# Kernel tuning notes

Measured on AMD Instinct MI355X. Metric: run time of the kernel, lower is better.

Reference implementation:

```python
import jax, jax.numpy as jnp
import numpy as np

B, T, E, H = 8, 2048, 1024, 64

def setup_inputs() -> dict:
    key = jax.random.key(0)
    kx, kq, kk, kv = jax.random.split(key, 4)
    x = jax.random.normal(kx, (B, T, E), dtype=jnp.float32)
    # torch Linear(E, H, bias=False): weight [H, E]; store transposed [E, H]
    scale = 1.0 / np.sqrt(E)
    Wq = jax.random.uniform(kq, (E, H), dtype=jnp.float32, minval=-scale, maxval=scale)
    Wk = jax.random.uniform(kk, (E, H), dtype=jnp.float32, minval=-scale, maxval=scale)
    Wv = jax.random.uniform(kv, (E, H), dtype=jnp.float32, minval=-scale, maxval=scale)
    return {"x": x, "Wq": Wq, "Wk": Wk, "Wv": Wv}

def reference(x, Wq, Wk, Wv):
    # x: [B,T,E]
    q = x @ Wq  # [B,T,H]
    k = x @ Wk
    v = x @ Wv
    head_size = q.shape[-1]
    scores = jnp.einsum('bth,bsh->bts', q, k) * (head_size ** -0.5)  # [B,T,T]
    Tlen = x.shape[1]
    causal = jnp.tril(jnp.ones((Tlen, Tlen), dtype=bool))
    scores = jnp.where(causal, scores, -jnp.inf)
    weights = jax.nn.softmax(scores, axis=-1)
    # dropout p=0.0 -> identity
    out = jnp.einsum('bts,bsh->bth', weights, v)  # [B,T,H]
    return out
```

## Files before the change

### kernel.cpp

```cpp
#include <hip/hip_runtime.h>
#include <hip/hip_bf16.h>

#define B_  8
#define T_  2048
#define E_  1024
#define H_  64
#define BT_ (B_*T_)

typedef __attribute__((ext_vector_type(8))) __bf16 bf16x8;
typedef __attribute__((ext_vector_type(4))) float  f32x4;

__device__ __forceinline__ unsigned short f2bfu(float f) {
    union { float f; unsigned u; } v; v.f = f;
    unsigned r = v.u + 0x7fffu + ((v.u >> 16) & 1u);
    return (unsigned short)(r >> 16);
}

__global__ __launch_bounds__(256, 2)
void qkv_kernel(const float* __restrict__ x,
                const float* __restrict__ Wq,
                const float* __restrict__ Wk,
                const float* __restrict__ Wv,
                unsigned short* __restrict__ qb,
                unsigned short* __restrict__ kb,
                unsigned short* __restrict__ vtb)
{
    __shared__ unsigned short xs[64 * 40];
    __shared__ unsigned short wt[3][64 * 40];

    const int tid  = threadIdx.x;
    const int wave = tid >> 6;
    const int lane = tid & 63;
    const int quad = lane >> 4;
    const int col  = lane & 15;
    const long r0  = (long)blockIdx.x * 64;

    f32x4 acc[3][4];
#pragma unroll
    for (int m = 0; m < 3; ++m)
#pragma unroll
        for (int n = 0; n < 4; ++n)
            acc[m][n] = (f32x4){0.f, 0.f, 0.f, 0.f};

    const float* W[3] = {Wq, Wk, Wv};

    const int xrow = tid >> 2;
    const int xk   = (tid & 3) * 8;
    const int wk   = tid >> 3;
    const int wh   = (tid & 7) * 8;

    for (int k0 = 0; k0 < E_; k0 += 32) {
        const float* xp = x + (r0 + xrow) * E_ + k0 + xk;
        float4 f0 = ((const float4*)xp)[0];
        float4 f1 = ((const float4*)xp)[1];
        unsigned pack[4];
        pack[0] = f2bfu(f0.x) | ((unsigned)f2bfu(f0.y) << 16);
        pack[1] = f2bfu(f0.z) | ((unsigned)f2bfu(f0.w) << 16);
        pack[2] = f2bfu(f1.x) | ((unsigned)f2bfu(f1.y) << 16);
        pack[3] = f2bfu(f1.z) | ((unsigned)f2bfu(f1.w) << 16);

        float wg[3][8];
#pragma unroll
        for (int m = 0; m < 3; ++m) {
            const float* wp = W[m] + (long)(k0 + wk) * H_ + wh;
            float4 g0 = ((const float4*)wp)[0];
            float4 g1 = ((const float4*)wp)[1];
            wg[m][0]=g0.x; wg[m][1]=g0.y; wg[m][2]=g0.z; wg[m][3]=g0.w;
            wg[m][4]=g1.x; wg[m][5]=g1.y; wg[m][6]=g1.z; wg[m][7]=g1.w;
        }

        __syncthreads();

        *(uint4*)&xs[xrow * 40 + xk] = *(uint4*)pack;
#pragma unroll
        for (int m = 0; m < 3; ++m)
#pragma unroll
            for (int j = 0; j < 8; ++j)
                wt[m][(wh + j) * 40 + wk] = f2bfu(wg[m][j]);

        __syncthreads();

        bf16x8 af = *(const bf16x8*)&xs[(wave * 16 + col) * 40 + quad * 8];
#pragma unroll
        for (int m = 0; m < 3; ++m)
#pragma unroll
            for (int n = 0; n < 4; ++n) {
                bf16x8 bfg = *(const bf16x8*)&wt[m][(n * 16 + col) * 40 + quad * 8];
                acc[m][n] = __builtin_amdgcn_mfma_f32_16x16x32_bf16(af, bfg, acc[m][n], 0, 0, 0);
            }
    }

    const int bidx = (int)(r0 >> 11);
#pragma unroll
    for (int n = 0; n < 4; ++n) {
        int h = n * 16 + col;
#pragma unroll
        for (int r = 0; r < 4; ++r) {
            long t = r0 + wave * 16 + quad * 4 + r;
            qb[t * H_ + h] = f2bfu(acc[0][n][r] * 0.125f);
            kb[t * H_ + h] = f2bfu(acc[1][n][r]);
            vtb[((long)(bidx * H_ + h)) * T_ + (t & (T_ - 1))] = f2bfu(acc[2][n][r]);
        }
    }
}

#define TS 72

__global__ __launch_bounds__(256, 2)
void attn_kernel(const unsigned short* __restrict__ qb,
                 const unsigned short* __restrict__ kb,
                 const unsigned short* __restrict__ vtb,
                 float* __restrict__ out)
{
    __shared__ unsigned short qs[64 * TS];
    __shared__ unsigned short ks[64 * TS];
    __shared__ unsigned short vs[64 * TS];
    __shared__ unsigned short ps[4][16 * TS];

    const int tid  = threadIdx.x;
    const int wave = tid >> 6;
    const int lane = tid & 63;
    const int quad = lane >> 4;
    const int col  = lane & 15;
    const int qt   = blockIdx.x & 31;
    const int b    = blockIdx.x >> 5;

    {
        const uint4* src = (const uint4*)(qb + ((long)b * T_ + qt * 64) * H_);
#pragma unroll
        for (int i = 0; i < 2; ++i) {
            int idx = tid + i * 256;
            int row = idx >> 3, c = idx & 7;
            *(uint4*)&qs[row * TS + c * 8] = src[idx];
        }
    }

    f32x4 o[4];
    float m_i[4], l_i[4];
#pragma unroll
    for (int n = 0; n < 4; ++n) o[n] = (f32x4){0.f, 0.f, 0.f, 0.f};
#pragma unroll
    for (int r = 0; r < 4; ++r) { m_i[r] = -1e30f; l_i[r] = 0.f; }

    for (int s = 0; s <= qt; ++s) {
        {
            const uint4* ksrc = (const uint4*)(kb + ((long)b * T_ + s * 64) * H_);
#pragma unroll
            for (int i = 0; i < 2; ++i) {
                int idx = tid + i * 256;
                int row = idx >> 3, c = idx & 7;
                *(uint4*)&ks[row * TS + c * 8] = ksrc[idx];
                const uint4* vsrc =
                    (const uint4*)(vtb + ((long)(b * H_ + row)) * T_ + s * 64) + c;
                *(uint4*)&vs[row * TS + c * 8] = *vsrc;
            }
        }
        __syncthreads();

        bf16x8 qa0 = *(const bf16x8*)&qs[(wave * 16 + col) * TS + quad * 8];
        bf16x8 qa1 = *(const bf16x8*)&qs[(wave * 16 + col) * TS + quad * 8 + 32];
        f32x4 sa[4];
#pragma unroll
        for (int kt = 0; kt < 4; ++kt) {
            bf16x8 kf0 = *(const bf16x8*)&ks[(kt * 16 + col) * TS + quad * 8];
            bf16x8 kf1 = *(const bf16x8*)&ks[(kt * 16 + col) * TS + quad * 8 + 32];
            sa[kt] = (f32x4){0.f, 0.f, 0.f, 0.f};
            sa[kt] = __builtin_amdgcn_mfma_f32_16x16x32_bf16(qa0, kf0, sa[kt], 0, 0, 0);
            sa[kt] = __builtin_amdgcn_mfma_f32_16x16x32_bf16(qa1, kf1, sa[kt], 0, 0, 0);
        }

        if (s == qt) {
#pragma unroll
            for (int kt = 0; kt < 4; ++kt) {
                int kg = kt * 16 + col;
#pragma unroll
                for (int r = 0; r < 4; ++r) {
                    int qg = wave * 16 + quad * 4 + r;
                    if (kg > qg) sa[kt][r] = -1e30f;
                }
            }
        }

        float mx[4];
#pragma unroll
        for (int r = 0; r < 4; ++r)
            mx[r] = fmaxf(fmaxf(sa[0][r], sa[1][r]), fmaxf(sa[2][r], sa[3][r]));
#pragma unroll
        for (int off = 1; off < 16; off <<= 1)
#pragma unroll
            for (int r = 0; r < 4; ++r)
                mx[r] = fmaxf(mx[r], __shfl_xor(mx[r], off, 64));

        float alpha[4], mnew[4];
#pragma unroll
        for (int r = 0; r < 4; ++r) {
            mnew[r]  = fmaxf(m_i[r], mx[r]);
            alpha[r] = __builtin_amdgcn_exp2f((m_i[r] - mnew[r]) * 1.44269504f);
            m_i[r]   = mnew[r];
        }

        float rs[4] = {0.f, 0.f, 0.f, 0.f};
#pragma unroll
        for (int kt = 0; kt < 4; ++kt)
#pragma unroll
            for (int r = 0; r < 4; ++r) {
                float p = __builtin_amdgcn_exp2f((sa[kt][r] - mnew[r]) * 1.44269504f);
                rs[r] += p;
                ps[wave][(quad * 4 + r) * TS + kt * 16 + col] = f2bfu(p);
            }
#pragma unroll
        for (int off = 1; off < 16; off <<= 1)
#pragma unroll
            for (int r = 0; r < 4; ++r)
                rs[r] += __shfl_xor(rs[r], off, 64);
#pragma unroll
        for (int r = 0; r < 4; ++r)
            l_i[r] = l_i[r] * alpha[r] + rs[r];

#pragma unroll
        for (int n = 0; n < 4; ++n)
#pragma unroll
            for (int r = 0; r < 4; ++r)
                o[n][r] *= alpha[r];

        bf16x8 pa0 = *(const bf16x8*)&ps[wave][col * TS + quad * 8];
        bf16x8 pa1 = *(const bf16x8*)&ps[wave][col * TS + quad * 8 + 32];
#pragma unroll
        for (int n = 0; n < 4; ++n) {
            bf16x8 vf0 = *(const bf16x8*)&vs[(n * 16 + col) * TS + quad * 8];
            bf16x8 vf1 = *(const bf16x8*)&vs[(n * 16 + col) * TS + quad * 8 + 32];
            o[n] = __builtin_amdgcn_mfma_f32_16x16x32_bf16(pa0, vf0, o[n], 0, 0, 0);
            o[n] = __builtin_amdgcn_mfma_f32_16x16x32_bf16(pa1, vf1, o[n], 0, 0, 0);
        }
        __syncthreads();
    }

#pragma unroll
    for (int r = 0; r < 4; ++r) {
        float inv = 1.0f / l_i[r];
        long row = (long)b * T_ + qt * 64 + wave * 16 + quad * 4 + r;
#pragma unroll
        for (int n = 0; n < 4; ++n)
            out[row * H_ + n * 16 + col] = o[n][r] * inv;
    }
}

extern "C" void kernel_launch(void* const* d_in, const int* in_sizes, int n_in,
                              void* d_out, int out_size, void* d_ws, size_t ws_size,
                              hipStream_t stream) {
    (void)in_sizes; (void)n_in; (void)out_size; (void)ws_size;
    const float* x  = (const float*)d_in[0];
    const float* Wq = (const float*)d_in[1];
    const float* Wk = (const float*)d_in[2];
    const float* Wv = (const float*)d_in[3];

    unsigned short* qb  = (unsigned short*)d_ws;
    unsigned short* kb  = qb + (size_t)BT_ * H_;
    unsigned short* vtb = kb + (size_t)BT_ * H_;

    qkv_kernel<<<BT_ / 64, 256, 0, stream>>>(x, Wq, Wk, Wv, qb, kb, vtb);
    attn_kernel<<<B_ * (T_ / 64), 256, 0, stream>>>(qb, kb, vtb, (float*)d_out);
}
```

Before: 195.7 us.

## Pre-convert weights to bf16, shrink QKV and attention tiles for more blocks

Result: slower. 245.5 us (+25.4%).

```diff
diff --git a/kernel.cpp b/kernel.cpp
--- a/kernel.cpp
+++ b/kernel.cpp
@@ -16,120 +16,104 @@
     return (unsigned short)(r >> 16);
 }
 
-__global__ __launch_bounds__(256, 2)
+__global__ __launch_bounds__(256)
+void wprep_kernel(const float* __restrict__ Wq,
+                  const float* __restrict__ Wk,
+                  const float* __restrict__ Wv,
+                  unsigned short* __restrict__ wtb)
+{
+    const int mat = blockIdx.x >> 6;
+    const int h   = blockIdx.x & 63;
+    const float* W = (mat == 0) ? Wq : (mat == 1 ? Wk : Wv);
+    unsigned short* row = wtb + ((long)(mat * 64 + h)) * E_;
+    const int e0 = threadIdx.x * 4;
+    unsigned p0 = f2bfu(W[(e0 + 0) * H_ + h]) | ((unsigned)f2bfu(W[(e0 + 1) * H_ + h]) << 16);
+    unsigned p1 = f2bfu(W[(e0 + 2) * H_ + h]) | ((unsigned)f2bfu(W[(e0 + 3) * H_ + h]) << 16);
+    *(uint2*)&row[e0] = (uint2){p0, p1};
+}
+
+__global__ __launch_bounds__(256, 4)
 void qkv_kernel(const float* __restrict__ x,
-                const float* __restrict__ Wq,
-                const float* __restrict__ Wk,
-                const float* __restrict__ Wv,
+                const unsigned short* __restrict__ wtb,
                 unsigned short* __restrict__ qb,
                 unsigned short* __restrict__ kb,
                 unsigned short* __restrict__ vtb)
 {
-    __shared__ unsigned short xs[64 * 40];
-    __shared__ unsigned short wt[3][64 * 40];
+    __shared__ unsigned short xs[2][16 * 72];
 
     const int tid  = threadIdx.x;
     const int wave = tid >> 6;
     const int lane = tid & 63;
     const int quad = lane >> 4;
     const int col  = lane & 15;
-    const long r0  = (long)blockIdx.x * 64;
-
-    f32x4 acc[3][4];
-#pragma unroll
-    for (int m = 0; m < 3; ++m)
-#pragma unroll
-        for (int n = 0; n < 4; ++n)
-            acc[m][n] = (f32x4){0.f, 0.f, 0.f, 0.f};
-
-    const float* W[3] = {Wq, Wk, Wv};
-
-    const int xrow = tid >> 2;
-    const int xk   = (tid & 3) * 8;
-    const int wk   = tid >> 3;
-    const int wh   = (tid & 7) * 8;
-
-    for (int k0 = 0; k0 < E_; k0 += 32) {
-        const float* xp = x + (r0 + xrow) * E_ + k0 + xk;
-        float4 f0 = ((const float4*)xp)[0];
-        float4 f1 = ((const float4*)xp)[1];
-        unsigned pack[4];
-        pack[0] = f2bfu(f0.x) | ((unsigned)f2bfu(f0.y) << 16);
-        pack[1] = f2bfu(f0.z) | ((unsigned)f2bfu(f0.w) << 16);
-        pack[2] = f2bfu(f1.x) | ((unsigned)f2bfu(f1.y) << 16);
-        pack[3] = f2bfu(f1.z) | ((unsigned)f2bfu(f1.w) << 16);
-
-        float wg[3][8];
-#pragma unroll
-        for (int m = 0; m < 3; ++m) {
-            const float* wp = W[m] + (long)(k0 + wk) * H_ + wh;
-            float4 g0 = ((const float4*)wp)[0];
-            float4 g1 = ((const float4*)wp)[1];
-            wg[m][0]=g0.x; wg[m][1]=g0.y; wg[m][2]=g0.z; wg[m][3]=g0.w;
-            wg[m][4]=g1.x; wg[m][5]=g1.y; wg[m][6]=g1.z; wg[m][7]=g1.w;
-        }
-
+    const long r0  = (long)blockIdx.x * 16;
+
+    f32x4 acc[3];
+#pragma unroll
+    for (int m = 0; m < 3; ++m) acc[m] = (f32x4){0.f, 0.f, 0.f, 0.f};
+
+    const int xrow = tid >> 4;
+    const int xkc  = (tid & 15) * 4;
+    const float* xbase = x + (r0 + xrow) * E_ + xkc;
+
+    float4 xv = *(const float4*)xbase;
+
+    for (int k0 = 0, it = 0; k0 < E_; k0 += 64, ++it) {
+        unsigned p0 = f2bfu(xv.x) | ((unsigned)f2bfu(xv.y) << 16);
+        unsigned p1 = f2bfu(xv.z) | ((unsigned)f2bfu(xv.w) << 16);
+        *(uint2*)&xs[it & 1][xrow * 72 + xkc] = (uint2){p0, p1};
         __syncthreads();
-
-        *(uint4*)&xs[xrow * 40 + xk] = *(uint4*)pack;
-#pragma unroll
-        for (int m = 0; m < 3; ++m)
-#pragma unroll
-            for (int j = 0; j < 8; ++j)
-                wt[m][(wh + j) * 40 + wk] = f2bfu(wg[m][j]);
-
-        __syncthreads();
-
-        bf16x8 af = *(const bf16x8*)&xs[(wave * 16 + col) * 40 + quad * 8];
-#pragma unroll
-        for (int m = 0; m < 3; ++m)
-#pragma unroll
-            for (int n = 0; n < 4; ++n) {
-                bf16x8 bfg = *(const bf16x8*)&wt[m][(n * 16 + col) * 40 + quad * 8];
-                acc[m][n] = __builtin_amdgcn_mfma_f32_16x16x32_bf16(af, bfg, acc[m][n], 0, 0, 0);
-            }
+        if (k0 + 64 < E_) xv = *(const float4*)(xbase + k0 + 64);
+
+#pragma unroll
+        for (int ks = 0; ks < 2; ++ks) {
+            bf16x8 af = *(const bf16x8*)&xs[it & 1][col * 72 + ks * 32 + quad * 8];
+            const int kk = k0 + ks * 32 + quad * 8;
+#pragma unroll
+            for (int m = 0; m < 3; ++m) {
+                bf16x8 bfg = *(const bf16x8*)&wtb[((long)(m * 64 + wave * 16 + col)) * E_ + kk];
+                acc[m] = __builtin_amdgcn_mfma_f32_16x16x32_bf16(af, bfg, acc[m], 0, 0, 0);
+            }
+        }
     }
 
     const int bidx = (int)(r0 >> 11);
-#pragma unroll
-    for (int n = 0; n < 4; ++n) {
-        int h = n * 16 + col;
-#pragma unroll
-        for (int r = 0; r < 4; ++r) {
-            long t = r0 + wave * 16 + quad * 4 + r;
-            qb[t * H_ + h] = f2bfu(acc[0][n][r] * 0.125f);
-            kb[t * H_ + h] = f2bfu(acc[1][n][r]);
-            vtb[((long)(bidx * H_ + h)) * T_ + (t & (T_ - 1))] = f2bfu(acc[2][n][r]);
-        }
+    const int h    = wave * 16 + col;
+#pragma unroll
+    for (int r = 0; r < 4; ++r) {
+        long t = r0 + quad * 4 + r;
+        qb[t * H_ + h] = f2bfu(acc[0][r] * 0.125f);
+        kb[t * H_ + h] = f2bfu(acc[1][r]);
+        vtb[((long)(bidx * H_ + h)) * T_ + (t & (T_ - 1))] = f2bfu(acc[2][r]);
     }
 }
 
 #define TS 72
 
-__global__ __launch_bounds__(256, 2)
+__global__ __launch_bounds__(128, 4)
 void attn_kernel(const unsigned short* __restrict__ qb,
                  const unsigned short* __restrict__ kb,
                  const unsigned short* __restrict__ vtb,
                  float* __restrict__ out)
 {
-    __shared__ unsigned short qs[64 * TS];
+    __shared__ unsigned short qs[32 * TS];
     __shared__ unsigned short ks[64 * TS];
     __shared__ unsigned short vs[64 * TS];
-    __shared__ unsigned short ps[4][16 * TS];
+    __shared__ unsigned short ps[2][16 * TS];
 
     const int tid  = threadIdx.x;
     const int wave = tid >> 6;
     const int lane = tid & 63;
     const int quad = lane >> 4;
     const int col  = lane & 15;
-    const int qt   = blockIdx.x & 31;
-    const int b    = blockIdx.x >> 5;
+    const int qt   = blockIdx.x & 63;
+    const int b    = blockIdx.x >> 6;
 
     {
-        const uint4* src = (const uint4*)(qb + ((long)b * T_ + qt * 64) * H_);
+        const uint4* src = (const uint4*)(qb + ((long)b * T_ + qt * 32) * H_);
 #pragma unroll
         for (int i = 0; i < 2; ++i) {
-            int idx = tid + i * 256;
+            int idx = tid + i * 128;
             int row = idx >> 3, c = idx & 7;
             *(uint4*)&qs[row * TS + c * 8] = src[idx];
         }
@@ -142,12 +126,13 @@
 #pragma unroll
     for (int r = 0; r < 4; ++r) { m_i[r] = -1e30f; l_i[r] = 0.f; }
 
-    for (int s = 0; s <= qt; ++s) {
+    const int nt = (qt >> 1) + 1;
+    for (int s = 0; s < nt; ++s) {
         {
             const uint4* ksrc = (const uint4*)(kb + ((long)b * T_ + s * 64) * H_);
 #pragma unroll
-            for (int i = 0; i < 2; ++i) {
-                int idx = tid + i * 256;
+            for (int i = 0; i < 4; ++i) {
+                int idx = tid + i * 128;
                 int row = idx >> 3, c = idx & 7;
                 *(uint4*)&ks[row * TS + c * 8] = ksrc[idx];
                 const uint4* vsrc =
@@ -169,13 +154,13 @@
             sa[kt] = __builtin_amdgcn_mfma_f32_16x16x32_bf16(qa1, kf1, sa[kt], 0, 0, 0);
         }
 
-        if (s == qt) {
+        if (s == nt - 1) {
 #pragma unroll
             for (int kt = 0; kt < 4; ++kt) {
-                int kg = kt * 16 + col;
+                int kg = s * 64 + kt * 16 + col;
 #pragma unroll
                 for (int r = 0; r < 4; ++r) {
-                    int qg = wave * 16 + quad * 4 + r;
+                    int qg = qt * 32 + wave * 16 + quad * 4 + r;
                     if (kg > qg) sa[kt][r] = -1e30f;
                 }
             }
@@ -238,7 +223,7 @@
 #pragma unroll
     for (int r = 0; r < 4; ++r) {
         float inv = 1.0f / l_i[r];
-        long row = (long)b * T_ + qt * 64 + wave * 16 + quad * 4 + r;
+        long row = (long)b * T_ + qt * 32 + wave * 16 + quad * 4 + r;
 #pragma unroll
         for (int n = 0; n < 4; ++n)
             out[row * H_ + n * 16 + col] = o[n][r] * inv;
@@ -257,7 +242,9 @@
     unsigned short* qb  = (unsigned short*)d_ws;
     unsigned short* kb  = qb + (size_t)BT_ * H_;
     unsigned short* vtb = kb + (size_t)BT_ * H_;
-
-    qkv_kernel<<<BT_ / 64, 256, 0, stream>>>(x, Wq, Wk, Wv, qb, kb, vtb);
-    attn_kernel<<<B_ * (T_ / 64), 256, 0, stream>>>(qb, kb, vtb, (float*)d_out);
-}
+    unsigned short* wtb = vtb + (size_t)BT_ * H_;
+
+    wprep_kernel<<<192, 256, 0, stream>>>(Wq, Wk, Wv, wtb);
+    qkv_kernel<<<BT_ / 16, 256, 0, stream>>>(x, wtb, qb, kb, vtb);
+    attn_kernel<<<B_ * (T_ / 32), 128, 0, stream>>>(qb, kb, vtb, (float*)d_out);
+}
```
